# Performance work log

Measured on AMD Instinct MI355X. Metric: run time of the kernel, lower is better.

The kernel has to match this reference:

```python
import jax, jax.numpy as jnp
import numpy as np

H = 16          # num_heads
KVH = 4         # num_kv_heads
HD = 128        # head_dim = dim // num_heads
BASE = 10000.0  # rope_base
EPS = 1.1920928955078125e-07  # torch F.rms_norm default eps = finfo(fp32).eps


def rotate_half(x):
    h = x.shape[-1] // 2
    return jnp.concatenate([-x[..., h:], x[..., :h]], axis=-1)


def rms_norm(x):
    return x * jax.lax.rsqrt(jnp.mean(x * x, axis=-1, keepdims=True) + EPS)


def setup_inputs() -> dict:
    key = jax.random.key(0)
    ks = jax.random.split(key, 5)
    D = H * HD
    KVD = KVH * HD
    s = 0.02
    x = jax.random.normal(ks[0], (4, 2048, D), jnp.float32)
    Wq = jax.random.normal(ks[1], (D, D), jnp.float32) * s
    Wk = jax.random.normal(ks[2], (KVD, D), jnp.float32) * s
    Wv = jax.random.normal(ks[3], (KVD, D), jnp.float32) * s
    Wproj = jax.random.normal(ks[4], (D, D), jnp.float32) * s
    q_gain = jnp.full((H,), 1.0, jnp.float32)
    return {"x": x, "Wq": Wq, "Wk": Wk, "Wv": Wv, "Wproj": Wproj, "q_gain": q_gain}


def reference(x, Wq, Wk, Wv, Wproj, q_gain):
    B, T, D = x.shape
    # QKV projections (bias-free), reshape to [B, heads, T, head_dim]
    q = (x @ Wq.T).reshape(B, T, H, HD).transpose(0, 2, 1, 3)
    k = (x @ Wk.T).reshape(B, T, KVH, HD).transpose(0, 2, 1, 3)
    v = (x @ Wv.T).reshape(B, T, KVH, HD).transpose(0, 2, 1, 3)
    # QK RMSNorm (no learned weight)
    q = rms_norm(q)
    k = rms_norm(k)
    # Rotary embedding tables [T, HD]
    t = jnp.arange(T, dtype=jnp.float32)
    inv_freq = 1.0 / (BASE ** (jnp.arange(0, HD, 2, dtype=jnp.float32) / HD))
    freqs = jnp.outer(t, inv_freq)
    emb = jnp.concatenate([freqs, freqs], axis=-1)
    cos, sin = jnp.cos(emb), jnp.sin(emb)
    # RoPE + per-head gain on q
    q = (q * cos + rotate_half(q) * sin) * q_gain[None, :, None, None]
    k = k * cos + rotate_half(k) * sin
    # GQA: repeat_interleave kv heads to match q heads
    groups = H // KVH
    k = jnp.repeat(k, groups, axis=1)
    v = jnp.repeat(v, groups, axis=1)
    # Causal scaled dot-product attention
    scores = jnp.einsum('bhqd,bhkd->bhqk', q, k) / np.float32(np.sqrt(HD))
    mask = jnp.tril(jnp.ones((T, T), dtype=bool))
    scores = jnp.where(mask, scores, -jnp.inf)
    attn = jax.nn.softmax(scores, axis=-1)
    y = jnp.einsum('bhqk,bhkd->bhqd', attn, v)
    y = y.transpose(0, 2, 1, 3).reshape(B, T, D)
    return y @ Wproj.T
```

## Files before the change

kernel.cpp:

```cpp
#include <hip/hip_runtime.h>
#include <math.h>


typedef float f32x4 __attribute__((ext_vector_type(4)));
typedef __bf16 bf16x8 __attribute__((ext_vector_type(8)));
typedef __bf16 bf16x4 __attribute__((ext_vector_type(4)));

__device__ __forceinline__ void load_lds16(const __bf16* g, __bf16* l) {
    __builtin_amdgcn_global_load_lds(
        (const __attribute__((address_space(1))) void*)g,
        (__attribute__((address_space(3))) void*)l, 16, 0, 0);
}

__global__ __launch_bounds__(256) void cvt_all(
    const float* __restrict__ x,  const float* __restrict__ Wq,
    const float* __restrict__ Wk, const float* __restrict__ Wv,
    const float* __restrict__ Wp, __bf16* __restrict__ dst)
{
    long long i = ((long long)blockIdx.x * 256 + threadIdx.x) * 4;
    if (i >= 27262976LL) return;
    const float* src;
    long long off;
    if (i < 16777216LL)      { src = x;  off = i; }
    else if (i < 20971520LL) { src = Wq; off = i - 16777216LL; }
    else if (i < 22020096LL) { src = Wk; off = i - 20971520LL; }
    else if (i < 23068672LL) { src = Wv; off = i - 22020096LL; }
    else                     { src = Wp; off = i - 23068672LL; }
    float4 v = *(const float4*)(src + off);
    bf16x4 o = {(__bf16)v.x, (__bf16)v.y, (__bf16)v.z, (__bf16)v.w};
    *(bf16x4*)(dst + i) = o;
}

template <int NI, typename OutT>
__global__ __launch_bounds__(512, 2) void gemm256(
    const __bf16* __restrict__ A, const __bf16* __restrict__ W,
    OutT* __restrict__ C, int M, int N, int K)
{
    constexpr int BN = 64 * NI;
    const int bn = blockIdx.x, bm = blockIdx.y;
    const int tid = threadIdx.x;
    const int lane = tid & 63;
    const int wave = tid >> 6;
    const int quad = lane >> 4, l16 = lane & 15;
    const int wm2 = wave >> 2;
    const int wn4 = wave & 3;

    __shared__ __bf16 As[2][256 * 64];
    __shared__ __bf16 Bs[2][BN * 64];

    f32x4 acc[8][NI] = {};

    const int sr = tid >> 3;
    const int sc = tid & 7;
    const int scs = sc ^ (sr & 7);

    const __bf16* Ag = A + (size_t)(bm * 256 + sr) * K + scs * 8;
    const __bf16* Wg = W + (size_t)(bn * BN + sr) * K + scs * 8;
    __bf16* Asd = &As[0][0] + sr * 64 + sc * 8;
    __bf16* Bsd = &Bs[0][0] + sr * 64 + sc * 8;

    auto stage = [&](int t, int h) {
        const int k0 = t * 64;
#pragma unroll
        for (int ra = 0; ra < 4; ++ra)
            load_lds16(Ag + (size_t)(ra * 64) * K + k0,
                       Asd + h * 16384 + ra * 4096);
#pragma unroll
        for (int rb = 0; rb < NI; ++rb)
            load_lds16(Wg + (size_t)(rb * 64) * K + k0,
                       Bsd + h * (BN * 64) + rb * 4096);
    };
    auto wait_prev = [&]() {
        if constexpr (NI == 4) asm volatile("s_waitcnt vmcnt(8)" ::: "memory");
        else                   asm volatile("s_waitcnt vmcnt(6)" ::: "memory");
    };

    const int NT = K / 64;

    stage(0, 0);
    stage(1, 1);
    wait_prev();
    asm volatile("" ::: "memory");
    __builtin_amdgcn_s_barrier();
    asm volatile("" ::: "memory");

    for (int t = 0; t < NT; ++t) {
        const int h = t & 1;
        const __bf16* Ab = &As[h][0];
        const __bf16* Bb = &Bs[h][0];

        bf16x8 bfr[NI][2];
#pragma unroll
        for (int ph = 0; ph < 4; ++ph) {
            bf16x8 af[2][2];
#pragma unroll
            for (int j = 0; j < 2; ++j)
#pragma unroll
                for (int ks = 0; ks < 2; ++ks)
                    af[j][ks] = *(const bf16x8*)(
                        Ab + (wm2 * 128 + (ph * 2 + j) * 16 + l16) * 64 +
                        (((ks * 4 + quad) ^ (l16 & 7)) * 8));
            if (ph == 0) {
#pragma unroll
                for (int ni = 0; ni < NI; ++ni)
#pragma unroll
                    for (int ks = 0; ks < 2; ++ks)
                        bfr[ni][ks] = *(const bf16x8*)(
                            Bb + (wn4 * 16 * NI + ni * 16 + l16) * 64 +
                            (((ks * 4 + quad) ^ (l16 & 7)) * 8));
            }
            asm volatile("" ::: "memory");
            __builtin_amdgcn_s_barrier();
            asm volatile("" ::: "memory");
            __builtin_amdgcn_s_setprio(1);
#pragma unroll
            for (int j = 0; j < 2; ++j)
#pragma unroll
                for (int ni = 0; ni < NI; ++ni)
#pragma unroll
                    for (int ks = 0; ks < 2; ++ks)
                        acc[ph * 2 + j][ni] = __builtin_amdgcn_mfma_f32_16x16x32_bf16(
                            af[j][ks], bfr[ni][ks], acc[ph * 2 + j][ni], 0, 0, 0);
            __builtin_amdgcn_s_setprio(0);
            asm volatile("" ::: "memory");
            __builtin_amdgcn_s_barrier();
            asm volatile("" ::: "memory");
        }

        if (t + 2 < NT) {
            stage(t + 2, h);
            wait_prev();
        } else if (t + 1 < NT) {
            asm volatile("s_waitcnt vmcnt(0)" ::: "memory");
        } else {
            break;
        }
        asm volatile("" ::: "memory");
        __builtin_amdgcn_s_barrier();
        asm volatile("" ::: "memory");
    }

#pragma unroll
    for (int mi = 0; mi < 8; ++mi) {
#pragma unroll
        for (int r = 0; r < 4; ++r) {
            int row = bm * 256 + wm2 * 128 + mi * 16 + quad * 4 + r;
            OutT* Cp = C + (size_t)row * N + bn * BN + wn4 * 16 * NI + l16;
#pragma unroll
            for (int ni = 0; ni < NI; ++ni)
                Cp[ni * 16] = (OutT)acc[mi][ni][r];
        }
    }
}

__global__ __launch_bounds__(256) void qk_norm_rope(
    __bf16* __restrict__ q, __bf16* __restrict__ kv,
    const float* __restrict__ q_gain)
{
    const int row = blockIdx.x * 4 + (threadIdx.x >> 6);
    const int lane = threadIdx.x & 63;
    const int BTH = 4 * 2048 * 16;

    __bf16* base;
    int t;
    float gain;
    if (row < BTH) {
        int bt = row >> 4, h = row & 15;
        base = q + (size_t)bt * 2048 + h * 128;
        t = bt & 2047;
        gain = q_gain[h];
    } else {
        int r2 = row - BTH;
        int bt = r2 >> 2, kvh = r2 & 3;
        base = kv + (size_t)bt * 1024 + kvh * 128;
        t = bt & 2047;
        gain = 1.0f;
    }

    float x0 = (float)base[lane];
    float x1 = (float)base[lane + 64];

    float ss = x0 * x0 + x1 * x1;
#pragma unroll
    for (int off = 32; off; off >>= 1) ss += __shfl_xor(ss, off);
    float inv = rsqrtf(ss * (1.0f / 128.0f) + 1.1920928955078125e-07f);
    x0 *= inv; x1 *= inv;

    float freq = exp2f(-(float)lane * 0.20762050593046013f);
    float ang = (float)t * freq;
    float s, c;
    sincosf(ang, &s, &c);
    float o0 = x0 * c - x1 * s;
    float o1 = x1 * c + x0 * s;
    base[lane]      = (__bf16)(o0 * gain);
    base[lane + 64] = (__bf16)(o1 * gain);
}

__global__ __launch_bounds__(256) void transpose_v(
    const __bf16* __restrict__ kv, __bf16* __restrict__ vtout)
{
    __shared__ __bf16 tile[64][65];
    const int b = blockIdx.z;
    const int t0 = blockIdx.x * 64, c0 = blockIdx.y * 64;
    const __bf16* vb = kv + (size_t)b * 2048 * 1024 + 512;
    __bf16* vtb = vtout + (size_t)b * 512 * 2048;
    const int j = threadIdx.x & 63;
    const int r0 = threadIdx.x >> 6;
#pragma unroll
    for (int i = 0; i < 16; ++i) {
        int r = r0 + i * 4;
        tile[r][j] = vb[(size_t)(t0 + r) * 1024 + c0 + j];
    }
    __syncthreads();
#pragma unroll
    for (int i = 0; i < 16; ++i) {
        int r = r0 + i * 4;
        vtb[(size_t)(c0 + r) * 2048 + t0 + j] = tile[j][r];
    }
}

__global__ __launch_bounds__(256, 2) void attn(
    const __bf16* __restrict__ q, const __bf16* __restrict__ kv,
    const __bf16* __restrict__ vt, __bf16* __restrict__ y,
    const float* __restrict__ q_gain)
{
    const int qt = 15 - blockIdx.y;
    const int bh = blockIdx.x;
    const int b = bh >> 4, h = bh & 15, kvh = h >> 2;
    const int tid = threadIdx.x;
    const int wave = tid >> 6, lane = tid & 63;
    const int quad = lane >> 4, l16 = lane & 15;

    __shared__ __bf16 Ks[2][64 * 128];
    __shared__ __bf16 Vts[2][128 * 64];
    __shared__ __bf16 Ps[2][4 * 16 * 64];

    const int qt0 = qt * 128;
    const int wq = wave * 16;

    bf16x8 qf[2][4];
#pragma unroll
    for (int p = 0; p < 2; ++p) {
        const size_t qrow =
            ((size_t)b * 2048 + qt0 + p * 64 + wq + l16) * 2048 + h * 128;
#pragma unroll
        for (int t = 0; t < 4; ++t)
            qf[p][t] = *(const bf16x8*)(q + qrow + t * 32 + quad * 8);
    }

    f32x4 oacc[2][8] = {};
    float lsum[2][4] = {};

    const float sm_scale = 0.12754635f;
    const float mfix = 11.5f * fabsf(q_gain[h]);

    const size_t kbase = (size_t)b * 2048 * 1024 + kvh * 128;
    const size_t vtbase = (size_t)(b * 4 + kvh) * 128 * 2048;

    const int rowK = lane >> 4, pcK = lane & 15;
    const int rowV = lane >> 3, pcV = lane & 7;

    const int nj = 2 * qt + 2;

    {
#pragma unroll
        for (int r = 0; r < 4; ++r) {
            int rrK = (r * 4 + wave) * 4 + rowK;
            int cK = pcK ^ (rrK & 15);
            load_lds16(kv + kbase + (size_t)rrK * 1024 + cK * 8,
                       &Ks[0][(r * 4 + wave) * 512]);
            int rrV = (r * 4 + wave) * 8 + rowV;
            int cV = pcV ^ (rrV & 7);
            load_lds16(vt + vtbase + (size_t)rrV * 2048 + cV * 8,
                       &Vts[0][(r * 4 + wave) * 512]);
        }
    }

    for (int jt = 0; jt < nj; ++jt) {
        const int cur = jt & 1;

        asm volatile("" ::: "memory");
        __builtin_amdgcn_s_barrier();
        asm volatile("" ::: "memory");

        if (jt + 1 < nj) {
            const int j0n = (jt + 1) * 64;
#pragma unroll
            for (int r = 0; r < 4; ++r) {
                int rrK = (r * 4 + wave) * 4 + rowK;
                int cK = pcK ^ (rrK & 15);
                load_lds16(kv + kbase + (size_t)(j0n + rrK) * 1024 + cK * 8,
                           &Ks[cur ^ 1][(r * 4 + wave) * 512]);
                int rrV = (r * 4 + wave) * 8 + rowV;
                int cV = pcV ^ (rrV & 7);
                load_lds16(vt + vtbase + (size_t)rrV * 2048 + j0n + cV * 8,
                           &Vts[cur ^ 1][(r * 4 + wave) * 512]);
            }
            asm volatile("s_waitcnt vmcnt(8)" ::: "memory");
        } else {
            asm volatile("s_waitcnt vmcnt(0)" ::: "memory");
        }

        asm volatile("" ::: "memory");
        __builtin_amdgcn_s_barrier();
        asm volatile("" ::: "memory");

        const __bf16* Kc = Ks[cur];
        const __bf16* Vc = Vts[cur];

        f32x4 sacc[2][4] = {};
        __builtin_amdgcn_s_setprio(1);
#pragma unroll
        for (int nt = 0; nt < 4; ++nt)
#pragma unroll
            for (int t = 0; t < 4; ++t) {
                bf16x8 kf = *(const bf16x8*)(
                    Kc + (nt * 16 + l16) * 128 + ((t * 4 + quad) ^ l16) * 8);
                sacc[0][nt] = __builtin_amdgcn_mfma_f32_16x16x32_bf16(
                    qf[0][t], kf, sacc[0][nt], 0, 0, 0);
                sacc[1][nt] = __builtin_amdgcn_mfma_f32_16x16x32_bf16(
                    qf[1][t], kf, sacc[1][nt], 0, 0, 0);
            }
        __builtin_amdgcn_s_setprio(0);

        if (jt >= 2 * qt) {
            const int dj = (jt - 2 * qt) * 64;
#pragma unroll
            for (int p = 0; p < 2; ++p) {
                const int rel = p * 64 + wq + quad * 4 - dj;
#pragma unroll
                for (int nt = 0; nt < 4; ++nt) {
                    int kg = nt * 16 + l16;
#pragma unroll
                    for (int r = 0; r < 4; ++r)
                        if (kg > rel + r) sacc[p][nt][r] = -3.0e38f;
                }
            }
        }

#pragma unroll
        for (int p = 0; p < 2; ++p) {
            __bf16* Pw = &Ps[p][0] + wave * 1024;
#pragma unroll
            for (int nt = 0; nt < 4; ++nt)
#pragma unroll
                for (int r = 0; r < 4; ++r) {
                    float pv = exp2f((sacc[p][nt][r] - mfix) * sm_scale);
                    lsum[p][r] += pv;
                    int row = quad * 4 + r;
                    int pc = (nt * 2 + (l16 >> 3)) ^ (row & 7);
                    Pw[row * 64 + pc * 8 + (l16 & 7)] = (__bf16)pv;
                }
        }

        __builtin_amdgcn_s_setprio(1);
#pragma unroll
        for (int kt = 0; kt < 2; ++kt) {
            const int pcc = ((kt * 4 + quad) ^ (l16 & 7)) * 8;
            bf16x8 pf0 = *(const bf16x8*)(&Ps[0][0] + wave * 1024 + l16 * 64 + pcc);
            bf16x8 pf1 = *(const bf16x8*)(&Ps[1][0] + wave * 1024 + l16 * 64 + pcc);
#pragma unroll
            for (int vn = 0; vn < 8; ++vn) {
                bf16x8 vf = *(const bf16x8*)(
                    Vc + (vn * 16 + l16) * 64 + pcc);
                oacc[0][vn] = __builtin_amdgcn_mfma_f32_16x16x32_bf16(
                    pf0, vf, oacc[0][vn], 0, 0, 0);
                oacc[1][vn] = __builtin_amdgcn_mfma_f32_16x16x32_bf16(
                    pf1, vf, oacc[1][vn], 0, 0, 0);
            }
        }
        __builtin_amdgcn_s_setprio(0);
    }

#pragma unroll
    for (int p = 0; p < 2; ++p) {
#pragma unroll
        for (int r = 0; r < 4; ++r)
#pragma unroll
            for (int off = 8; off; off >>= 1)
                lsum[p][r] += __shfl_xor(lsum[p][r], off);

        const size_t ybase =
            ((size_t)b * 2048 + qt0 + p * 64 + wq) * 2048 + h * 128;
#pragma unroll
        for (int r = 0; r < 4; ++r) {
            float inv = 1.0f / lsum[p][r];
            __bf16* yp = y + ybase + (size_t)(quad * 4 + r) * 2048 + l16;
#pragma unroll
            for (int vn = 0; vn < 8; ++vn)
                yp[vn * 16] = (__bf16)(oacc[p][vn][r] * inv);
        }
    }
}

extern "C" void kernel_launch(void* const* d_in, const int* in_sizes, int n_in,
                              void* d_out, int out_size, void* d_ws, size_t ws_size,
                              hipStream_t stream) {
    const float* x     = (const float*)d_in[0];
    const float* Wq    = (const float*)d_in[1];
    const float* Wk    = (const float*)d_in[2];
    const float* Wv    = (const float*)d_in[3];
    const float* Wproj = (const float*)d_in[4];
    const float* qgain = (const float*)d_in[5];
    float* outp = (float*)d_out;

    __bf16* xb  = (__bf16*)d_ws;
    __bf16* Wqb = xb  + 16777216;
    __bf16* Wkb = Wqb + 4194304;
    __bf16* Wvb = Wkb + 1048576;
    __bf16* Wpb = Wvb + 1048576;
    __bf16* q   = Wpb + 4194304;
    __bf16* kvb = q   + 16777216;
    __bf16* vt  = kvb + 8388608;
    __bf16* y   = q;

    dim3 blk(256);
    cvt_all<<<dim3(27262976 / 1024), blk, 0, stream>>>(x, Wq, Wk, Wv, Wproj, xb);

    gemm256<4, __bf16><<<dim3(8, 32), dim3(512), 0, stream>>>(xb, Wqb, q, 8192, 2048, 2048);
    gemm256<2, __bf16><<<dim3(8, 32), dim3(512), 0, stream>>>(xb, Wkb, kvb, 8192, 1024, 2048);
    qk_norm_rope<<<dim3((4 * 2048 * (16 + 4)) / 4), blk, 0, stream>>>(q, kvb, qgain);
    transpose_v<<<dim3(32, 8, 4), blk, 0, stream>>>(kvb, vt);
    attn<<<dim3(64, 16), blk, 0, stream>>>(q, kvb, vt, y, qgain);
    gemm256<4, float><<<dim3(8, 32), dim3(512), 0, stream>>>(y, Wpb, outp, 8192, 2048, 2048);
}
```

Measured before the change: 513.1 us.

## Triple-buffer GEMM with K-tile 32 and interleaved prefetch

Rewrites the bf16 GEMM used for the Q/K/V and output projections. It now uses a three-stage LDS ring with 32-wide K tiles instead of a two-stage ring with 64-wide tiles. Global-to-LDS prefetches for tile t+2 are issued between the LDS fragment reads of the current tile, and each iteration has one barrier instead of eight. The goal is to cut synchronisation overhead and overlap memory traffic with MFMA work. In exchange, each barrier covers half as much MFMA work, and the LDS swizzle is changed to a 4-chunk XOR pattern that could raise bank conflicts.

New measurement: 492.3 us. 1.04x faster.

```diff
diff --git a/kernel.cpp b/kernel.cpp
--- a/kernel.cpp
+++ b/kernel.cpp
@@ -32,11 +32,12 @@
 }
 
 template <int NI, typename OutT>
-__global__ __launch_bounds__(512, 2) void gemm256(
+__global__ __launch_bounds__(512, 2) void gemm3buf(
     const __bf16* __restrict__ A, const __bf16* __restrict__ W,
     OutT* __restrict__ C, int M, int N, int K)
 {
     constexpr int BN = 64 * NI;
+    constexpr int WN = 16 * NI;
     const int bn = blockIdx.x, bm = blockIdx.y;
     const int tid = threadIdx.x;
     const int lane = tid & 63;
@@ -45,99 +46,88 @@
     const int wm2 = wave >> 2;
     const int wn4 = wave & 3;
 
-    __shared__ __bf16 As[2][256 * 64];
-    __shared__ __bf16 Bs[2][BN * 64];
+    __shared__ __bf16 As[3][256 * 32];
+    __shared__ __bf16 Bs[3][BN * 32];
 
     f32x4 acc[8][NI] = {};
 
-    const int sr = tid >> 3;
-    const int sc = tid & 7;
-    const int scs = sc ^ (sr & 7);
+    const int sr = tid >> 2;
+    const int sc = tid & 3;
+    const int scs = sc ^ (sr & 3) ^ ((sr >> 2) & 3);
+    const int swzq = quad ^ (l16 & 3) ^ ((l16 >> 2) & 3);
 
     const __bf16* Ag = A + (size_t)(bm * 256 + sr) * K + scs * 8;
     const __bf16* Wg = W + (size_t)(bn * BN + sr) * K + scs * 8;
-    __bf16* Asd = &As[0][0] + sr * 64 + sc * 8;
-    __bf16* Bsd = &Bs[0][0] + sr * 64 + sc * 8;
-
-    auto stage = [&](int t, int h) {
-        const int k0 = t * 64;
-#pragma unroll
-        for (int ra = 0; ra < 4; ++ra)
-            load_lds16(Ag + (size_t)(ra * 64) * K + k0,
-                       Asd + h * 16384 + ra * 4096);
-#pragma unroll
-        for (int rb = 0; rb < NI; ++rb)
-            load_lds16(Wg + (size_t)(rb * 64) * K + k0,
-                       Bsd + h * (BN * 64) + rb * 4096);
+    const int dA = sr * 32 + sc * 8;
+
+    auto stage = [&](int t, int buf) {
+        const int k0 = t * 32;
+        load_lds16(Ag + k0, &As[buf][dA]);
+        load_lds16(Ag + (size_t)128 * K + k0, &As[buf][128 * 32 + dA]);
+        load_lds16(Wg + k0, &Bs[buf][dA]);
+        if constexpr (NI == 4)
+            load_lds16(Wg + (size_t)128 * K + k0, &Bs[buf][128 * 32 + dA]);
     };
-    auto wait_prev = [&]() {
-        if constexpr (NI == 4) asm volatile("s_waitcnt vmcnt(8)" ::: "memory");
-        else                   asm volatile("s_waitcnt vmcnt(6)" ::: "memory");
+    auto wait_cnt = [&]() {
+        if constexpr (NI == 4) asm volatile("s_waitcnt vmcnt(4)" ::: "memory");
+        else                   asm volatile("s_waitcnt vmcnt(3)" ::: "memory");
     };
 
-    const int NT = K / 64;
+    const int NT = K / 32;
 
     stage(0, 0);
     stage(1, 1);
-    wait_prev();
+    wait_cnt();
     asm volatile("" ::: "memory");
     __builtin_amdgcn_s_barrier();
     asm volatile("" ::: "memory");
 
+    int cur = 0, nb = 2;
     for (int t = 0; t < NT; ++t) {
-        const int h = t & 1;
-        const __bf16* Ab = &As[h][0];
-        const __bf16* Bb = &Bs[h][0];
-
-        bf16x8 bfr[NI][2];
-#pragma unroll
-        for (int ph = 0; ph < 4; ++ph) {
-            bf16x8 af[2][2];
-#pragma unroll
-            for (int j = 0; j < 2; ++j)
-#pragma unroll
-                for (int ks = 0; ks < 2; ++ks)
-                    af[j][ks] = *(const bf16x8*)(
-                        Ab + (wm2 * 128 + (ph * 2 + j) * 16 + l16) * 64 +
-                        (((ks * 4 + quad) ^ (l16 & 7)) * 8));
-            if (ph == 0) {
-#pragma unroll
-                for (int ni = 0; ni < NI; ++ni)
-#pragma unroll
-                    for (int ks = 0; ks < 2; ++ks)
-                        bfr[ni][ks] = *(const bf16x8*)(
-                            Bb + (wn4 * 16 * NI + ni * 16 + l16) * 64 +
-                            (((ks * 4 + quad) ^ (l16 & 7)) * 8));
-            }
+        const __bf16* Ab = &As[cur][0];
+        const __bf16* Bb = &Bs[cur][0];
+        const bool pf = (t + 2 < NT);
+        const int k0n = (t + 2) * 32;
+
+        bf16x8 bfr[NI];
+#pragma unroll
+        for (int ni = 0; ni < NI; ++ni)
+            bfr[ni] = *(const bf16x8*)(
+                Bb + (wn4 * WN + ni * 16 + l16) * 32 + swzq * 8);
+        if (pf) {
+            load_lds16(Wg + k0n, &Bs[nb][dA]);
+            if constexpr (NI == 4)
+                load_lds16(Wg + (size_t)128 * K + k0n, &Bs[nb][128 * 32 + dA]);
+        }
+
+        bf16x8 af[8];
+#pragma unroll
+        for (int mi = 0; mi < 8; ++mi)
+            af[mi] = *(const bf16x8*)(
+                Ab + (wm2 * 128 + mi * 16 + l16) * 32 + swzq * 8);
+        if (pf) {
+            load_lds16(Ag + k0n, &As[nb][dA]);
+            load_lds16(Ag + (size_t)128 * K + k0n, &As[nb][128 * 32 + dA]);
+        }
+
+        __builtin_amdgcn_s_setprio(1);
+#pragma unroll
+        for (int mi = 0; mi < 8; ++mi)
+#pragma unroll
+            for (int ni = 0; ni < NI; ++ni)
+                acc[mi][ni] = __builtin_amdgcn_mfma_f32_16x16x32_bf16(
+                    af[mi], bfr[ni], acc[mi][ni], 0, 0, 0);
+        __builtin_amdgcn_s_setprio(0);
+
+        if (t + 1 < NT) {
+            if (pf) wait_cnt();
+            else    asm volatile("s_waitcnt vmcnt(0)" ::: "memory");
             asm volatile("" ::: "memory");
             __builtin_amdgcn_s_barrier();
             asm volatile("" ::: "memory");
-            __builtin_amdgcn_s_setprio(1);
-#pragma unroll
-            for (int j = 0; j < 2; ++j)
-#pragma unroll
-                for (int ni = 0; ni < NI; ++ni)
-#pragma unroll
-                    for (int ks = 0; ks < 2; ++ks)
-                        acc[ph * 2 + j][ni] = __builtin_amdgcn_mfma_f32_16x16x32_bf16(
-                            af[j][ks], bfr[ni][ks], acc[ph * 2 + j][ni], 0, 0, 0);
-            __builtin_amdgcn_s_setprio(0);
-            asm volatile("" ::: "memory");
-            __builtin_amdgcn_s_barrier();
-            asm volatile("" ::: "memory");
-        }
-
-        if (t + 2 < NT) {
-            stage(t + 2, h);
-            wait_prev();
-        } else if (t + 1 < NT) {
-            asm volatile("s_waitcnt vmcnt(0)" ::: "memory");
-        } else {
-            break;
-        }
-        asm volatile("" ::: "memory");
-        __builtin_amdgcn_s_barrier();
-        asm volatile("" ::: "memory");
+        }
+        cur = (cur + 1 == 3) ? 0 : cur + 1;
+        nb  = (nb  + 1 == 3) ? 0 : nb + 1;
     }
 
 #pragma unroll
@@ -145,7 +135,7 @@
 #pragma unroll
         for (int r = 0; r < 4; ++r) {
             int row = bm * 256 + wm2 * 128 + mi * 16 + quad * 4 + r;
-            OutT* Cp = C + (size_t)row * N + bn * BN + wn4 * 16 * NI + l16;
+            OutT* Cp = C + (size_t)row * N + bn * BN + wn4 * WN + l16;
 #pragma unroll
             for (int ni = 0; ni < NI; ++ni)
                 Cp[ni * 16] = (OutT)acc[mi][ni][r];
@@ -417,10 +407,10 @@
     dim3 blk(256);
     cvt_all<<<dim3(27262976 / 1024), blk, 0, stream>>>(x, Wq, Wk, Wv, Wproj, xb);
 
-    gemm256<4, __bf16><<<dim3(8, 32), dim3(512), 0, stream>>>(xb, Wqb, q, 8192, 2048, 2048);
-    gemm256<2, __bf16><<<dim3(8, 32), dim3(512), 0, stream>>>(xb, Wkb, kvb, 8192, 1024, 2048);
+    gemm3buf<4, __bf16><<<dim3(8, 32), dim3(512), 0, stream>>>(xb, Wqb, q, 8192, 2048, 2048);
+    gemm3buf<2, __bf16><<<dim3(8, 32), dim3(512), 0, stream>>>(xb, Wkb, kvb, 8192, 1024, 2048);
     qk_norm_rope<<<dim3((4 * 2048 * (16 + 4)) / 4), blk, 0, stream>>>(q, kvb, qgain);
     transpose_v<<<dim3(32, 8, 4), blk, 0, stream>>>(kvb, vt);
     attn<<<dim3(64, 16), blk, 0, stream>>>(q, kvb, vt, y, qgain);
-    gemm256<4, float><<<dim3(8, 32), dim3(512), 0, stream>>>(y, Wpb, outp, 8192, 2048, 2048);
-}
+    gemm3buf<4, float><<<dim3(8, 32), dim3(512), 0, stream>>>(y, Wpb, outp, 8192, 2048, 2048);
+}
```
